# Kernel optimization log

Measured on AMD Instinct MI355X. Metric: run time of the kernel, lower is better.

Reference implementation:

```python
import jax, jax.numpy as jnp
import numpy as np

# SLAYER SRM-ALPHA neuron / simulation constants (from netParams)
THETA = 10.0      # spike threshold
TAU_SR = 10.0     # PSP (SRM) time constant
TAU_REF = 1.0     # refractory time constant
SCALE_REF = 2.0
TAU_RHO = 1.0     # surrogate-gradient width (unused in fwd)
SCALE_RHO = 1.0
TS = 1.0
K_SRM = 100       # truncation of alpha kernel (values < 1e-4 beyond this)
K_REF = 16

def _alpha_kernel(tau, K, mult):
    t = jnp.arange(K, dtype=jnp.float32) * TS
    return mult * (t / tau) * jnp.exp(1.0 - t / tau)

SRM_KERNEL = _alpha_kernel(TAU_SR, K_SRM, 1.0)                       # eps(t)
REF_KERNEL = _alpha_kernel(TAU_REF, K_REF, -2.0 * THETA * SCALE_REF)  # nu(t)

def heaviside(u):
    return (u >= THETA).astype(u.dtype)

def psp(x):
    # causal temporal convolution with SRM alpha kernel; x: (..., T)
    T = x.shape[-1]
    K = SRM_KERNEL.shape[0]
    flat = x.reshape(-1, 1, T)  # (N, C=1, T)
    out = jax.lax.conv_general_dilated(flat, SRM_KERNEL[::-1].reshape(1, 1, K),
                                       (1,), [(K - 1, 0)])
    return out.reshape(x.shape)

def spike(v):
    # SLAYER spike generation with refractory feedback; v: (..., T)
    refk = REF_KERNEL[1:]          # refractory affects strictly future steps
    L = refk.shape[0]
    vT = jnp.moveaxis(v, -1, 0)    # (T, ...)
    pend0 = jnp.zeros(vT.shape[1:] + (L,), v.dtype)  # pending refractory contributions
    def step(pend, vt):
        u = vt + pend[..., 0]
        s = heaviside(u)
        pend = jnp.concatenate([pend[..., 1:], jnp.zeros_like(pend[..., :1])], axis=-1) \
               + s[..., None] * refk
        return pend, s
    _, sT = jax.lax.scan(step, pend0, vT)
    return jnp.moveaxis(sT, 0, -1)

def conv_t(x, W, pad):
    # per-timestep 2D conv (slayer.conv uses Conv3d with kernel (k,k,1), no bias)
    B, C, H, Wd, T = x.shape
    xt = jnp.transpose(x, (0, 4, 1, 2, 3)).reshape(B * T, C, H, Wd)
    y = jax.lax.conv_general_dilated(xt, W, (1, 1), [(pad, pad), (pad, pad)])
    Co, Ho, Wo = y.shape[1:]
    return jnp.transpose(y.reshape(B, T, Co, Ho, Wo), (0, 2, 3, 4, 1))

def pool_t(x):
    # slayer.pool(2): 2x2 sum-pool with constant weight 1.1*theta per element
    s = jax.lax.reduce_window(x, 0.0, jax.lax.add, (1, 1, 2, 2, 1), (1, 1, 2, 2, 1), 'VALID')
    return s * (1.1 * THETA)

def _forward(spikeInput, W1, W2, W3, W4, Wfc):
    x = spike(conv_t(psp(spikeInput), W1, 1))   # (B,16,48,48,T)
    x = spike(pool_t(psp(x)))                   # (B,16,24,24,T)
    x = spike(conv_t(psp(x), W2, 1))            # (B,32,24,24,T)
    x = spike(pool_t(psp(x)))                   # (B,32,12,12,T)
    x = spike(conv_t(psp(x), W3, 1))            # (B,64,12,12,T)
    x = spike(pool_t(psp(x)))                   # (B,64,6,6,T)
    x = spike(conv_t(psp(x), W4, 1))            # (B,64,6,6,T)
    x = spike(jnp.einsum('bchwt,kchw->bkt', psp(x), Wfc))  # (B,10,T)
    return x

def setup_inputs():
    key = jax.random.key(0)
    ks = jax.random.split(key, 6)
    B, T = 4, 200
    spikeInput = (jax.random.uniform(ks[0], (B, 2, 50, 50, T)) < 0.05).astype(jnp.float32)
    W1 = 0.5 * jax.random.normal(ks[1], (16, 2, 5, 5), jnp.float32)
    W2 = 0.25 * jax.random.normal(ks[2], (32, 16, 3, 3), jnp.float32)
    W3 = 0.25 * jax.random.normal(ks[3], (64, 32, 3, 3), jnp.float32)
    W4 = 0.25 * jax.random.normal(ks[4], (64, 64, 3, 3), jnp.float32)
    Wfc = 0.1 * jax.random.normal(ks[5], (10, 64, 6, 6), jnp.float32)
    return {"spikeInput": spikeInput, "W1": W1, "W2": W2, "W3": W3, "W4": W4, "Wfc": Wfc}

def reference(spikeInput, W1, W2, W3, W4, Wfc):
    return _forward(spikeInput, W1, W2, W3, W4, Wfc)
```

## Files before the change

kernel.cpp:

```cpp
#include <hip/hip_runtime.h>
#include <math.h>


#define THETA 10.0f
#define RSTRIDE 204

__global__ void prep_kernel(const float* __restrict__ W1, const float* __restrict__ W2,
                            const float* __restrict__ W3, const float* __restrict__ W4,
                            float* HQ, float* rk,
                            float* wt1, float* wt2, float* wt3, float* wt4) {
    int i = blockIdx.x * 256 + threadIdx.x;
    if (i < 144) {
        int k = i - 15;
        float val = 0.0f;
        if (k >= 0 && k <= 99) {
            float tf = (float)k;
            float x = tf / 10.0f;
            val = x * (float)exp((double)(1.0f - x));
        }
        HQ[i] = val;
    } else if (i < 160) {
        int j = i - 144;
        if (j < 15) {
            float t = (float)(j + 1);
            rk[j] = (-40.0f * t) * (float)exp((double)(1.0f - t));
        }
    } else if (i < 960) {
        int j = i - 160, co = j / 50, tp = j % 50;
        wt1[tp * 16 + co] = W1[j];
    } else if (i < 5568) {
        int j = i - 960, co = j / 144, tp = j % 144;
        wt2[tp * 32 + co] = W2[j];
    } else if (i < 24000) {
        int j = i - 5568, co = j / 288, tp = j % 288;
        wt3[tp * 64 + co] = W3[j];
    } else if (i < 60864) {
        int j = i - 24000, co = j / 576, tp = j % 576;
        wt4[tp * 64 + co] = W4[j];
    }
}

#define FIR_STEP(A0, A1, A2, A3, qx, qy, qz, qw, hA, hB)  \
    A0 = fmaf(hA.x, qw, A0);                              \
    A1 = fmaf(hA.y, qw, A1);                              \
    A2 = fmaf(hA.z, qw, A2);                              \
    A3 = fmaf(hA.w, qw, A3);                              \
    A0 = fmaf(hA.y, qz, A0);                              \
    A1 = fmaf(hA.z, qz, A1);                              \
    A2 = fmaf(hA.w, qz, A2);                              \
    A3 = fmaf(hB.x, qz, A3);                              \
    A0 = fmaf(hA.z, qy, A0);                              \
    A1 = fmaf(hA.w, qy, A1);                              \
    A2 = fmaf(hB.x, qy, A2);                              \
    A3 = fmaf(hB.y, qy, A3);                              \
    A0 = fmaf(hA.w, qx, A0);                              \
    A1 = fmaf(hB.x, qx, A1);                              \
    A2 = fmaf(hB.y, qx, A2);                              \
    A3 = fmaf(hB.z, qx, A3);

#define SCAN4(XV, p, rk)                                          \
    {                                                             \
        float u_, sv_;                                            \
        u_ = XV.x + p[0]; sv_ = (u_ >= THETA) ? 1.0f : 0.0f;      \
        XV.x = sv_;                                               \
        _Pragma("unroll")                                         \
        for (int i_ = 0; i_ < 14; ++i_) p[i_] = fmaf(sv_, rk[i_], p[i_ + 1]); \
        p[14] = sv_ * rk[14];                                     \
        u_ = XV.y + p[0]; sv_ = (u_ >= THETA) ? 1.0f : 0.0f;      \
        XV.y = sv_;                                               \
        _Pragma("unroll")                                         \
        for (int i_ = 0; i_ < 14; ++i_) p[i_] = fmaf(sv_, rk[i_], p[i_ + 1]); \
        p[14] = sv_ * rk[14];                                     \
        u_ = XV.z + p[0]; sv_ = (u_ >= THETA) ? 1.0f : 0.0f;      \
        XV.z = sv_;                                               \
        _Pragma("unroll")                                         \
        for (int i_ = 0; i_ < 14; ++i_) p[i_] = fmaf(sv_, rk[i_], p[i_ + 1]); \
        p[14] = sv_ * rk[14];                                     \
        u_ = XV.w + p[0]; sv_ = (u_ >= THETA) ? 1.0f : 0.0f;      \
        XV.w = sv_;                                               \
        _Pragma("unroll")                                         \
        for (int i_ = 0; i_ < 14; ++i_) p[i_] = fmaf(sv_, rk[i_], p[i_ + 1]); \
        p[14] = sv_ * rk[14];                                     \
    }

template <int NSUB>
__device__ __forceinline__ void fir_run(const float* __restrict__ row,
                                        const float4* __restrict__ HQ4,
                                        int t0, int jend, float4 (&acc)[NSUB]) {
    float4 H[5];
    #pragma unroll
    for (int m = 0; m < 5; ++m) H[m] = HQ4[m];
    const float* bp = row + t0 + 4 * (NSUB - 1);
    for (int j = 0; j <= jend; ++j) {
        const float4 qv = *reinterpret_cast<const float4*>(bp);
        const float4 Hn = HQ4[j + 5];
        #pragma unroll
        for (int d = 0; d < NSUB; ++d) {
            const float4 hA = H[d + 4 - NSUB];
            const float4 hB = H[d + 5 - NSUB];
            FIR_STEP(acc[d].x, acc[d].y, acc[d].z, acc[d].w,
                     qv.x, qv.y, qv.z, qv.w, hA, hB)
        }
        #pragma unroll
        for (int m = 0; m < 4; ++m) H[m] = H[m + 1];
        H[4] = Hn;
        bp -= 4;
    }
}

template <bool SCAN>
__global__ __launch_bounds__(512) void spikepsp_kernel(const float* __restrict__ in,
                                                       float* __restrict__ out,
                                                       const float* __restrict__ HQ,
                                                       const float* __restrict__ rkt,
                                                       int n) {
    __shared__ __align__(16) float tile[64 * RSTRIDE];
    const int l = threadIdx.x & 63;
    const int w = threadIdx.x >> 6;
    const int s0 = blockIdx.x * 64;
    for (int i = threadIdx.x; i < 3200; i += 512) {
        const int slot = i / 50, q = i - slot * 50;
        const int ser = s0 + slot;
        float4 v = make_float4(0.f, 0.f, 0.f, 0.f);
        if (ser < n) v = *reinterpret_cast<const float4*>(in + (long)ser * 200 + 4 * q);
        *reinterpret_cast<float4*>(&tile[slot * RSTRIDE + 4 * q]) = v;
    }
    __syncthreads();
    if (SCAN) {
        if (w == 0) {
            float rk[15];
            #pragma unroll
            for (int i = 0; i < 15; ++i) rk[i] = rkt[i];
            float p[15];
            #pragma unroll
            for (int i = 0; i < 15; ++i) p[i] = 0.0f;
            float* row = tile + l * RSTRIDE;
            for (int tq = 0; tq < 50; ++tq) {
                float4 xv = *reinterpret_cast<const float4*>(&row[4 * tq]);
                SCAN4(xv, p, rk)
                *reinterpret_cast<float4*>(&row[4 * tq]) = xv;
            }
        }
        __syncthreads();
    }
    const bool valid = (s0 + l) < n;
    const float* row = tile + l * RSTRIDE;
    const float4* HQ4 = reinterpret_cast<const float4*>(HQ);
    float* op = out + (long)(s0 + l) * 200;
    for (int item = w; item < 13; item += 8) {
        if (item < 12) {
            const int t0 = 16 * item;
            const int gm = (4 * item < 25) ? 4 * item : 25;
            float4 acc[4];
            #pragma unroll
            for (int d = 0; d < 4; ++d) acc[d] = make_float4(0.f, 0.f, 0.f, 0.f);
            fir_run<4>(row, HQ4, t0, gm + 3, acc);
            if (valid) {
                #pragma unroll
                for (int d = 0; d < 4; ++d)
                    *reinterpret_cast<float4*>(op + t0 + 4 * d) = acc[d];
            }
        } else {
            float4 acc[2];
            #pragma unroll
            for (int d = 0; d < 2; ++d) acc[d] = make_float4(0.f, 0.f, 0.f, 0.f);
            fir_run<2>(row, HQ4, 192, 26, acc);
            if (valid) {
                #pragma unroll
                for (int d = 0; d < 2; ++d)
                    *reinterpret_cast<float4*>(op + 192 + 4 * d) = acc[d];
            }
        }
    }
}

__global__ __launch_bounds__(512) void spikepsppool_kernel(const float* __restrict__ in,
                                                           float* __restrict__ out,
                                                           const float* __restrict__ HQ,
                                                           const float* __restrict__ rkt,
                                                           int C, int HO, int WO) {
    __shared__ __align__(16) float tile[64 * RSTRIDE];
    __shared__ int sbase[64];
    const int l = threadIdx.x & 63;
    const int w = threadIdx.x >> 6;
    const int o0 = blockIdx.x * 16;
    const int H = 2 * HO, W = 2 * WO;
    if (threadIdx.x < 64) {
        const int oi = threadIdx.x >> 2, p = threadIdx.x & 3;
        const int o = o0 + oi;
        const int wo = o % WO; int tmp = o / WO;
        const int ho = tmp % HO; tmp /= HO;
        const int c = tmp % C; const int b = tmp / C;
        sbase[threadIdx.x] = ((b * C + c) * H + 2 * ho + (p >> 1)) * W + 2 * wo + (p & 1);
    }
    __syncthreads();
    for (int i = threadIdx.x; i < 3200; i += 512) {
        const int slot = i / 50, q = i - slot * 50;
        const float4 v = *reinterpret_cast<const float4*>(in + (long)sbase[slot] * 200 + 4 * q);
        *reinterpret_cast<float4*>(&tile[slot * RSTRIDE + 4 * q]) = v;
    }
    __syncthreads();
    if (w == 0) {
        float rk[15];
        #pragma unroll
        for (int i = 0; i < 15; ++i) rk[i] = rkt[i];
        float p[15];
        #pragma unroll
        for (int i = 0; i < 15; ++i) p[i] = 0.0f;
        float* row = tile + l * RSTRIDE;
        for (int tq = 0; tq < 50; ++tq) {
            float4 xv = *reinterpret_cast<const float4*>(&row[4 * tq]);
            SCAN4(xv, p, rk)
            *reinterpret_cast<float4*>(&row[4 * tq]) = xv;
        }
    }
    __syncthreads();
    const int qb = l & ~3;
    const float* row = tile + l * RSTRIDE;
    const float4* HQ4 = reinterpret_cast<const float4*>(HQ);
    float* op = out + (long)(o0 + (l >> 2)) * 200;
    auto qsum = [&](float v) -> float {
        const float v0 = __shfl(v, qb + 0);
        const float v1 = __shfl(v, qb + 1);
        const float v2 = __shfl(v, qb + 2);
        const float v3 = __shfl(v, qb + 3);
        return (((v0 + v1) + v2) + v3) * 11.0f;
    };
    for (int item = w; item < 13; item += 8) {
        if (item < 12) {
            const int t0 = 16 * item;
            const int gm = (4 * item < 25) ? 4 * item : 25;
            float4 acc[4];
            #pragma unroll
            for (int d = 0; d < 4; ++d) acc[d] = make_float4(0.f, 0.f, 0.f, 0.f);
            fir_run<4>(row, HQ4, t0, gm + 3, acc);
            #pragma unroll
            for (int d = 0; d < 4; ++d) {
                float4 r;
                r.x = qsum(acc[d].x); r.y = qsum(acc[d].y);
                r.z = qsum(acc[d].z); r.w = qsum(acc[d].w);
                if ((l & 3) == 0)
                    *reinterpret_cast<float4*>(op + t0 + 4 * d) = r;
            }
        } else {
            float4 acc[2];
            #pragma unroll
            for (int d = 0; d < 2; ++d) acc[d] = make_float4(0.f, 0.f, 0.f, 0.f);
            fir_run<2>(row, HQ4, 192, 26, acc);
            #pragma unroll
            for (int d = 0; d < 2; ++d) {
                float4 r;
                r.x = qsum(acc[d].x); r.y = qsum(acc[d].y);
                r.z = qsum(acc[d].z); r.w = qsum(acc[d].w);
                if ((l & 3) == 0)
                    *reinterpret_cast<float4*>(op + 192 + 4 * d) = r;
            }
        }
    }
}

template <int K, int PAD, int CI, int COG>
__global__ __launch_bounds__(256) void conv_kernel(const float* __restrict__ x,
                                                   const float* __restrict__ wt,
                                                   float* __restrict__ out,
                                                   int Co, int H, int W,
                                                   int HO, int WO) {
    const int l = threadIdx.x & 63;
    const int wv = threadIdx.x >> 6;
    if (l >= 50) return;
    const int p = blockIdx.x * 4 + wv;
    const int wo = p % WO, ho = p / WO;
    const int co0 = blockIdx.y * COG;
    const int b = blockIdx.z;
    const int t0 = l * 4;
    float4 acc[COG];
    #pragma unroll
    for (int c = 0; c < COG; ++c) acc[c] = make_float4(0.f, 0.f, 0.f, 0.f);
    const float* xb = x + ((long)b * CI * H * W) * 200 + t0;
    for (int ci = 0; ci < CI; ++ci) {
        #pragma unroll
        for (int kh = 0; kh < K; ++kh) {
            const int hi = ho + kh - PAD;
            if (hi < 0 || hi >= H) continue;
            #pragma unroll
            for (int kw = 0; kw < K; ++kw) {
                const int wi = wo + kw - PAD;
                if (wi < 0 || wi >= W) continue;
                const float4 v = *reinterpret_cast<const float4*>(
                    xb + ((long)(ci * H + hi) * W + wi) * 200);
                const float* wp = wt + ((ci * K + kh) * K + kw) * Co + co0;
                #pragma unroll
                for (int c = 0; c < COG; ++c) {
                    const float wv_ = wp[c];
                    acc[c].x = fmaf(wv_, v.x, acc[c].x);
                    acc[c].y = fmaf(wv_, v.y, acc[c].y);
                    acc[c].z = fmaf(wv_, v.z, acc[c].z);
                    acc[c].w = fmaf(wv_, v.w, acc[c].w);
                }
            }
        }
    }
    const long hwN = (long)HO * WO;
    const long ob = ((long)(b * Co + co0) * HO + ho) * WO + wo;
    #pragma unroll
    for (int c = 0; c < COG; ++c)
        *reinterpret_cast<float4*>(out + (ob + c * hwN) * 200 + t0) = acc[c];
}

template <int CI, int COG>
__global__ __launch_bounds__(256) void conv3_kernel(const float* __restrict__ x,
                                                    const float* __restrict__ wt,
                                                    float* __restrict__ out,
                                                    int Co, int H, int W) {
    const int l = threadIdx.x & 63;
    const int wv = threadIdx.x >> 6;
    if (l >= 50) return;
    const int p = blockIdx.x * 4 + wv;
    const int wo = p % W, ho = p / W;
    const int co0 = blockIdx.y * COG;
    const int b = blockIdx.z;
    const int t0 = l * 4;
    float4 acc[COG];
    #pragma unroll
    for (int c = 0; c < COG; ++c) acc[c] = make_float4(0.f, 0.f, 0.f, 0.f);

    bool vm[9];
    #pragma unroll
    for (int i = 0; i < 9; ++i) {
        const int hi = ho + i / 3 - 1, wi = wo + i % 3 - 1;
        vm[i] = (hi >= 0) && (hi < H) && (wi >= 0) && (wi < W);
    }
    const long cis = (long)H * W * 200;
    const float* pb = x + (long)b * CI * cis + ((long)(ho - 1) * W + (wo - 1)) * 200 + t0;

    float4 bufA[9], bufB[9];
    auto ld = [&](int ci, float4 (&B)[9]) {
        const float* pc = pb + ci * cis;
        #pragma unroll
        for (int i = 0; i < 9; ++i) {
            B[i] = vm[i] ? *reinterpret_cast<const float4*>(pc + ((i / 3) * W + (i % 3)) * 200)
                         : make_float4(0.f, 0.f, 0.f, 0.f);
        }
    };
    auto fm = [&](const float4 (&B)[9], int ci) {
        #pragma unroll
        for (int i = 0; i < 9; ++i) {
            const float* wp = wt + (ci * 9 + i) * Co + co0;
            #pragma unroll
            for (int c = 0; c < COG; ++c) {
                const float wv_ = wp[c];
                acc[c].x = fmaf(wv_, B[i].x, acc[c].x);
                acc[c].y = fmaf(wv_, B[i].y, acc[c].y);
                acc[c].z = fmaf(wv_, B[i].z, acc[c].z);
                acc[c].w = fmaf(wv_, B[i].w, acc[c].w);
            }
        }
    };

    ld(0, bufA);
    #pragma unroll 1
    for (int ci = 0; ci < CI; ci += 2) {
        ld(ci + 1, bufB);
        fm(bufA, ci);
        if (ci + 2 < CI) ld(ci + 2, bufA);
        fm(bufB, ci + 1);
    }

    const long hwN = (long)H * W;
    const long ob = ((long)(b * Co + co0) * H + ho) * W + wo;
    #pragma unroll
    for (int c = 0; c < COG; ++c)
        *reinterpret_cast<float4*>(out + (ob + c * hwN) * 200 + t0) = acc[c];
}

__global__ __launch_bounds__(256) void spike_kernel(const float* __restrict__ v,
                                                    float* __restrict__ s,
                                                    const float* __restrict__ rkt,
                                                    int n) {
    const int nid = blockIdx.x * 256 + threadIdx.x;
    if (nid >= n) return;
    float rk[15];
    #pragma unroll
    for (int i = 0; i < 15; ++i) rk[i] = rkt[i];
    float p[15];
    #pragma unroll
    for (int i = 0; i < 15; ++i) p[i] = 0.0f;
    const float* vp = v + (long)nid * 200;
    float* sp = s + (long)nid * 200;
    for (int t = 0; t < 200; ++t) {
        const float u = vp[t] + p[0];
        const float sv = (u >= THETA) ? 1.0f : 0.0f;
        sp[t] = sv;
        #pragma unroll
        for (int i = 0; i < 14; ++i) p[i] = fmaf(sv, rk[i], p[i + 1]);
        p[14] = sv * rk[14];
    }
}

__global__ __launch_bounds__(64) void fc_kernel(const float* __restrict__ x,
                                                const float* __restrict__ wf,
                                                float* __restrict__ out) {
    __shared__ __align__(16) float xs[2304 * 8];
    const int b = blockIdx.x;
    const int t0 = blockIdx.y * 8;
    const int l = threadIdx.x;
    const float* xb = x + (long)b * 2304 * 200 + t0;
    for (int i = l; i < 4608; i += 64) {
        const int m = i >> 1, q = i & 1;
        const float4 v = *reinterpret_cast<const float4*>(xb + (long)m * 200 + 4 * q);
        *reinterpret_cast<float4*>(&xs[m * 8 + 4 * q]) = v;
    }
    __syncthreads();
    if (l < 20) {
        const int k = l >> 1, q = l & 1;
        float4 acc = make_float4(0.f, 0.f, 0.f, 0.f);
        const float* wp = wf + k * 2304;
        const float* xp = xs + 4 * q;
        for (int m = 0; m < 2304; ++m) {
            const float4 v = *reinterpret_cast<const float4*>(xp + m * 8);
            const float wv_ = wp[m];
            acc.x = fmaf(wv_, v.x, acc.x);
            acc.y = fmaf(wv_, v.y, acc.y);
            acc.z = fmaf(wv_, v.z, acc.z);
            acc.w = fmaf(wv_, v.w, acc.w);
        }
        *reinterpret_cast<float4*>(out + ((long)b * 10 + k) * 200 + t0 + 4 * q) = acc;
    }
}

extern "C" void kernel_launch(void* const* d_in, const int* in_sizes, int n_in,
                              void* d_out, int out_size, void* d_ws, size_t ws_size,
                              hipStream_t stream) {
    const float* x_in = (const float*)d_in[0];
    const float* W1 = (const float*)d_in[1];
    const float* W2 = (const float*)d_in[2];
    const float* W3 = (const float*)d_in[3];
    const float* W4 = (const float*)d_in[4];
    const float* Wfc = (const float*)d_in[5];
    float* outp = (float*)d_out;

    float* ws = (float*)d_ws;
    float* HQ  = ws;
    float* rk  = ws + 144;
    float* wt1 = ws + 160;
    float* wt2 = wt1 + 800;
    float* wt3 = wt2 + 4608;
    float* wt4 = wt3 + 18432;
    float* A   = wt4 + 36864;
    float* B   = A + 7372800;
    float* C   = B + 29491200;

    hipLaunchKernelGGL(prep_kernel, dim3(238), dim3(256), 0, stream,
                       W1, W2, W3, W4, HQ, rk, wt1, wt2, wt3, wt4);

    hipLaunchKernelGGL((spikepsp_kernel<false>), dim3(313), dim3(512), 0, stream,
                       x_in, A, HQ, rk, 20000);
    hipLaunchKernelGGL((conv_kernel<5, 1, 2, 16>), dim3(2304 / 4, 1, 4), dim3(256), 0, stream,
                       A, wt1, B, 16, 50, 50, 48, 48);
    hipLaunchKernelGGL(spikepsppool_kernel, dim3(36864 / 16), dim3(512), 0, stream,
                       B, A, HQ, rk, 16, 24, 24);
    hipLaunchKernelGGL((spikepsp_kernel<true>), dim3(36864 / 64), dim3(512), 0, stream,
                       A, B, HQ, rk, 36864);
    hipLaunchKernelGGL((conv3_kernel<16, 8>), dim3(576 / 4, 4, 4), dim3(256), 0, stream,
                       B, wt2, C, 32, 24, 24);
    hipLaunchKernelGGL(spikepsppool_kernel, dim3(18432 / 16), dim3(512), 0, stream,
                       C, A, HQ, rk, 32, 12, 12);
    hipLaunchKernelGGL((spikepsp_kernel<true>), dim3(18432 / 64), dim3(512), 0, stream,
                       A, B, HQ, rk, 18432);
    hipLaunchKernelGGL((conv3_kernel<32, 8>), dim3(144 / 4, 8, 4), dim3(256), 0, stream,
                       B, wt3, C, 64, 12, 12);
    hipLaunchKernelGGL(spikepsppool_kernel, dim3(9216 / 16), dim3(512), 0, stream,
                       C, A, HQ, rk, 64, 6, 6);
    hipLaunchKernelGGL((spikepsp_kernel<true>), dim3(9216 / 64), dim3(512), 0, stream,
                       A, B, HQ, rk, 9216);
    hipLaunchKernelGGL((conv3_kernel<64, 4>), dim3(36 / 4, 16, 4), dim3(256), 0, stream,
                       B, wt4, C, 64, 6, 6);
    hipLaunchKernelGGL((spikepsp_kernel<true>), dim3(9216 / 64), dim3(512), 0, stream,
                       C, B, HQ, rk, 9216);
    hipLaunchKernelGGL(fc_kernel, dim3(4, 25), dim3(64), 0, stream, B, Wfc, A);
    hipLaunchKernelGGL(spike_kernel, dim3(1), dim3(256), 0, stream, A, outp, rk, 40);
    (void)in_sizes; (void)n_in; (void)out_size; (void)ws_size;
}
```

Before: 705.6 us.

## Rebalance PSP FIR work across waves and parallelize FC over timesteps

```diff
diff --git a/kernel.cpp b/kernel.cpp
--- a/kernel.cpp
+++ b/kernel.cpp
@@ -83,30 +83,26 @@
         p[14] = sv_ * rk[14];                                     \
     }
 
-template <int NSUB>
-__device__ __forceinline__ void fir_run(const float* __restrict__ row,
-                                        const float4* __restrict__ HQ4,
-                                        int t0, int jend, float4 (&acc)[NSUB]) {
-    float4 H[5];
-    #pragma unroll
-    for (int m = 0; m < 5; ++m) H[m] = HQ4[m];
-    const float* bp = row + t0 + 4 * (NSUB - 1);
+__device__ __forceinline__ void fir_run2(const float* __restrict__ row,
+                                         const float4* __restrict__ HQ4,
+                                         int t0, int jend, float4 (&acc)[2]) {
+    float4 A = HQ4[2], B = HQ4[3], C = HQ4[4];
+    const float* bp = row + t0 + 4;
     for (int j = 0; j <= jend; ++j) {
         const float4 qv = *reinterpret_cast<const float4*>(bp);
-        const float4 Hn = HQ4[j + 5];
-        #pragma unroll
-        for (int d = 0; d < NSUB; ++d) {
-            const float4 hA = H[d + 4 - NSUB];
-            const float4 hB = H[d + 5 - NSUB];
-            FIR_STEP(acc[d].x, acc[d].y, acc[d].z, acc[d].w,
-                     qv.x, qv.y, qv.z, qv.w, hA, hB)
-        }
-        #pragma unroll
-        for (int m = 0; m < 4; ++m) H[m] = H[m + 1];
-        H[4] = Hn;
+        const float4 N = HQ4[j + 5];
+        FIR_STEP(acc[0].x, acc[0].y, acc[0].z, acc[0].w,
+                 qv.x, qv.y, qv.z, qv.w, A, B)
+        FIR_STEP(acc[1].x, acc[1].y, acc[1].z, acc[1].w,
+                 qv.x, qv.y, qv.z, qv.w, B, C)
+        A = B; B = C; C = N;
         bp -= 4;
     }
 }
+
+__device__ static const signed char FIR_ITEMS[8][4] = {
+    {24, 12, 8, -1}, {22, 21, 4, -1}, {20, 19, 3, -1}, {18, 17, 2, -1},
+    {16, 15, 1, 0},  {13, 11, 5, -1}, {14, 10, 6, -1}, {23, 9, 7, -1}};
 
 template <bool SCAN>
 __global__ __launch_bounds__(512) void spikepsp_kernel(const float* __restrict__ in,
@@ -147,29 +143,19 @@
     const float* row = tile + l * RSTRIDE;
     const float4* HQ4 = reinterpret_cast<const float4*>(HQ);
     float* op = out + (long)(s0 + l) * 200;
-    for (int item = w; item < 13; item += 8) {
-        if (item < 12) {
-            const int t0 = 16 * item;
-            const int gm = (4 * item < 25) ? 4 * item : 25;
-            float4 acc[4];
-            #pragma unroll
-            for (int d = 0; d < 4; ++d) acc[d] = make_float4(0.f, 0.f, 0.f, 0.f);
-            fir_run<4>(row, HQ4, t0, gm + 3, acc);
-            if (valid) {
-                #pragma unroll
-                for (int d = 0; d < 4; ++d)
-                    *reinterpret_cast<float4*>(op + t0 + 4 * d) = acc[d];
-            }
-        } else {
-            float4 acc[2];
-            #pragma unroll
-            for (int d = 0; d < 2; ++d) acc[d] = make_float4(0.f, 0.f, 0.f, 0.f);
-            fir_run<2>(row, HQ4, 192, 26, acc);
-            if (valid) {
-                #pragma unroll
-                for (int d = 0; d < 2; ++d)
-                    *reinterpret_cast<float4*>(op + 192 + 4 * d) = acc[d];
-            }
+    #pragma unroll
+    for (int k = 0; k < 4; ++k) {
+        const int id = FIR_ITEMS[w][k];
+        if (id < 0) break;
+        const int t0 = 8 * id;
+        const int jend = ((2 * id < 25) ? 2 * id : 25) + 1;
+        float4 acc[2];
+        acc[0] = make_float4(0.f, 0.f, 0.f, 0.f);
+        acc[1] = make_float4(0.f, 0.f, 0.f, 0.f);
+        fir_run2(row, HQ4, t0, jend, acc);
+        if (valid) {
+            *reinterpret_cast<float4*>(op + t0) = acc[0];
+            *reinterpret_cast<float4*>(op + t0 + 4) = acc[1];
         }
     }
 }
@@ -226,35 +212,23 @@
         const float v3 = __shfl(v, qb + 3);
         return (((v0 + v1) + v2) + v3) * 11.0f;
     };
-    for (int item = w; item < 13; item += 8) {
-        if (item < 12) {
-            const int t0 = 16 * item;
-            const int gm = (4 * item < 25) ? 4 * item : 25;
-            float4 acc[4];
-            #pragma unroll
-            for (int d = 0; d < 4; ++d) acc[d] = make_float4(0.f, 0.f, 0.f, 0.f);
-            fir_run<4>(row, HQ4, t0, gm + 3, acc);
-            #pragma unroll
-            for (int d = 0; d < 4; ++d) {
-                float4 r;
-                r.x = qsum(acc[d].x); r.y = qsum(acc[d].y);
-                r.z = qsum(acc[d].z); r.w = qsum(acc[d].w);
-                if ((l & 3) == 0)
-                    *reinterpret_cast<float4*>(op + t0 + 4 * d) = r;
-            }
-        } else {
-            float4 acc[2];
-            #pragma unroll
-            for (int d = 0; d < 2; ++d) acc[d] = make_float4(0.f, 0.f, 0.f, 0.f);
-            fir_run<2>(row, HQ4, 192, 26, acc);
-            #pragma unroll
-            for (int d = 0; d < 2; ++d) {
-                float4 r;
-                r.x = qsum(acc[d].x); r.y = qsum(acc[d].y);
-                r.z = qsum(acc[d].z); r.w = qsum(acc[d].w);
-                if ((l & 3) == 0)
-                    *reinterpret_cast<float4*>(op + 192 + 4 * d) = r;
-            }
+    #pragma unroll
+    for (int k = 0; k < 4; ++k) {
+        const int id = FIR_ITEMS[w][k];
+        if (id < 0) break;
+        const int t0 = 8 * id;
+        const int jend = ((2 * id < 25) ? 2 * id : 25) + 1;
+        float4 acc[2];
+        acc[0] = make_float4(0.f, 0.f, 0.f, 0.f);
+        acc[1] = make_float4(0.f, 0.f, 0.f, 0.f);
+        fir_run2(row, HQ4, t0, jend, acc);
+        #pragma unroll
+        for (int d = 0; d < 2; ++d) {
+            float4 r;
+            r.x = qsum(acc[d].x); r.y = qsum(acc[d].y);
+            r.z = qsum(acc[d].z); r.w = qsum(acc[d].w);
+            if ((l & 3) == 0)
+                *reinterpret_cast<float4*>(op + t0 + 4 * d) = r;
         }
     }
 }
@@ -397,34 +371,37 @@
     }
 }
 
-__global__ __launch_bounds__(64) void fc_kernel(const float* __restrict__ x,
-                                                const float* __restrict__ wf,
-                                                float* __restrict__ out) {
-    __shared__ __align__(16) float xs[2304 * 8];
+__global__ __launch_bounds__(128) void fc_kernel(const float* __restrict__ x,
+                                                 const float* __restrict__ wf,
+                                                 float* __restrict__ out) {
+    __shared__ __align__(16) float xs[8 * 2308];
     const int b = blockIdx.x;
     const int t0 = blockIdx.y * 8;
-    const int l = threadIdx.x;
+    const int tid = threadIdx.x;
     const float* xb = x + (long)b * 2304 * 200 + t0;
-    for (int i = l; i < 4608; i += 64) {
-        const int m = i >> 1, q = i & 1;
-        const float4 v = *reinterpret_cast<const float4*>(xb + (long)m * 200 + 4 * q);
-        *reinterpret_cast<float4*>(&xs[m * 8 + 4 * q]) = v;
+    for (int i = tid; i < 4608; i += 128) {
+        const int m = i >> 1, qh = (i & 1) * 4;
+        const float4 v = *reinterpret_cast<const float4*>(xb + (long)m * 200 + qh);
+        xs[(qh + 0) * 2308 + m] = v.x;
+        xs[(qh + 1) * 2308 + m] = v.y;
+        xs[(qh + 2) * 2308 + m] = v.z;
+        xs[(qh + 3) * 2308 + m] = v.w;
     }
     __syncthreads();
-    if (l < 20) {
-        const int k = l >> 1, q = l & 1;
-        float4 acc = make_float4(0.f, 0.f, 0.f, 0.f);
+    if (tid < 80) {
+        const int k = tid >> 3, q = tid & 7;
+        float a = 0.0f;
         const float* wp = wf + k * 2304;
-        const float* xp = xs + 4 * q;
-        for (int m = 0; m < 2304; ++m) {
-            const float4 v = *reinterpret_cast<const float4*>(xp + m * 8);
-            const float wv_ = wp[m];
-            acc.x = fmaf(wv_, v.x, acc.x);
-            acc.y = fmaf(wv_, v.y, acc.y);
-            acc.z = fmaf(wv_, v.z, acc.z);
-            acc.w = fmaf(wv_, v.w, acc.w);
-        }
-        *reinterpret_cast<float4*>(out + ((long)b * 10 + k) * 200 + t0 + 4 * q) = acc;
+        const float* xp = xs + q * 2308;
+        for (int m4 = 0; m4 < 2304; m4 += 4) {
+            const float4 xv = *reinterpret_cast<const float4*>(xp + m4);
+            const float4 wv = *reinterpret_cast<const float4*>(wp + m4);
+            a = fmaf(wv.x, xv.x, a);
+            a = fmaf(wv.y, xv.y, a);
+            a = fmaf(wv.z, xv.z, a);
+            a = fmaf(wv.w, xv.w, a);
+        }
+        out[((long)b * 10 + k) * 200 + t0 + q] = a;
     }
 }
 
@@ -477,7 +454,7 @@
                        B, wt4, C, 64, 6, 6);
     hipLaunchKernelGGL((spikepsp_kernel<true>), dim3(9216 / 64), dim3(512), 0, stream,
                        C, B, HQ, rk, 9216);
-    hipLaunchKernelGGL(fc_kernel, dim3(4, 25), dim3(64), 0, stream, B, Wfc, A);
+    hipLaunchKernelGGL(fc_kernel, dim3(4, 25), dim3(128), 0, stream, B, Wfc, A);
     hipLaunchKernelGGL(spike_kernel, dim3(1), dim3(256), 0, stream, A, outp, rk, 40);
     (void)in_sizes; (void)n_in; (void)out_size; (void)ws_size;
 }
```

Measured after the change: 674.8 us. -4.4%, faster.
